# Performance work log

Measured on AMD Instinct MI355X. Metric: run time of the kernel, lower is better.

Reference implementation:

```python
import jax, jax.numpy as jnp
import numpy as np

H = 32  # hidden_size

def _lstm_cell(x, h, c, Wih, Whh, bih, bhh):
    # PyTorch LSTMCell: gates order i, f, g, o
    g = x @ Wih.T + bih + h @ Whh.T + bhh  # [B, 4H]
    i, f, gg, o = jnp.split(g, 4, axis=-1)
    i = jax.nn.sigmoid(i); f = jax.nn.sigmoid(f)
    gg = jnp.tanh(gg);     o = jax.nn.sigmoid(o)
    c_new = f * c + i * gg
    h_new = o * jnp.tanh(c_new)
    return h_new, c_new


def setup_inputs() -> dict:
    key = jax.random.key(0)
    ks = jax.random.split(key, 16)
    B, T, I = 16384, 32, 27
    s_ih0 = 1.0 / np.sqrt(H)
    inp = {
        "obscured_tensor": jax.random.uniform(ks[0], (B, T, I), dtype=jnp.float32),
        "guessed_tensor": jax.random.uniform(ks[1], (B, 26), dtype=jnp.float32),
        # init_state uses xavier_normal on [B,H]: std = sqrt(2/(B+H))
        "h0": jax.random.normal(ks[2], (B, H), dtype=jnp.float32) * np.sqrt(2.0 / (B + H)),
        "c0": jax.random.normal(ks[3], (B, H), dtype=jnp.float32) * np.sqrt(2.0 / (B + H)),
        # layer 0 LSTMCell params (uniform(-1/sqrt(H), 1/sqrt(H)) like torch)
        "Wih0": jax.random.uniform(ks[4], (4 * H, I), jnp.float32, -s_ih0, s_ih0),
        "Whh0": jax.random.uniform(ks[5], (4 * H, H), jnp.float32, -s_ih0, s_ih0),
        "bih0": jax.random.uniform(ks[6], (4 * H,), jnp.float32, -s_ih0, s_ih0),
        "bhh0": jax.random.uniform(ks[7], (4 * H,), jnp.float32, -s_ih0, s_ih0),
        # layer 1 LSTMCell params
        "Wih1": jax.random.uniform(ks[8], (4 * H, H), jnp.float32, -s_ih0, s_ih0),
        "Whh1": jax.random.uniform(ks[9], (4 * H, H), jnp.float32, -s_ih0, s_ih0),
        "bih1": jax.random.uniform(ks[10], (4 * H,), jnp.float32, -s_ih0, s_ih0),
        "bhh1": jax.random.uniform(ks[11], (4 * H,), jnp.float32, -s_ih0, s_ih0),
        # fc: Linear(H + 26, 26)
        "Wfc": jax.random.uniform(ks[12], (26, H + 26), jnp.float32, -1.0 / np.sqrt(H + 26), 1.0 / np.sqrt(H + 26)),
        "bfc": jax.random.uniform(ks[13], (26,), jnp.float32, -1.0 / np.sqrt(H + 26), 1.0 / np.sqrt(H + 26)),
    }
    return inp


def reference(obscured_tensor, guessed_tensor, h0, c0,
              Wih0, Whh0, bih0, bhh0, Wih1, Whh1, bih1, bhh1, Wfc, bfc):
    B, T, _ = obscured_tensor.shape
    # faithful to torch: .view(T, B, -1) is a raw reshape, not a transpose
    xs = obscured_tensor.reshape(T, B, -1)  # [T, B, 27]

    def step(carry, x):
        h1, c1, h2, c2, hsum = carry
        h1, c1 = _lstm_cell(x, h1, c1, Wih0, Whh0, bih0, bhh0)
        h2, c2 = _lstm_cell(h1, h2, c2, Wih1, Whh1, bih1, bhh1)
        return (h1, c1, h2, c2, hsum + h2), None

    # init_state aliases the same xavier-initialized tensor for all layers
    init = (h0, c0, h0, c0, jnp.zeros_like(h0))
    (h1, c1, h2, c2, hsum), _ = jax.lax.scan(step, init, xs)

    # 'avg' aggregation: mean over time of concat(h_top, guessed);
    # guessed is time-constant so mean(concat) == concat(mean(h), guessed)
    agg = jnp.concatenate([hsum / T, guessed_tensor], axis=1)  # [B, H+26]
    logits = agg @ Wfc.T + bfc
    return logits, jax.nn.sigmoid(logits)
```

## Files before the change

### kernel.cpp

```cpp
#include <hip/hip_runtime.h>
#include <hip/hip_bf16.h>

#define NB 16384
#define NT 32
#define NI 27
#define NH 32
#define NG 26

typedef __attribute__((ext_vector_type(8))) short bf16x8;
typedef __attribute__((ext_vector_type(4))) float f32x4;
typedef __attribute__((ext_vector_type(4))) int   i32x4;

#define MFMA(a, b, c) __builtin_amdgcn_mfma_f32_16x16x32_bf16((a), (b), (c), 0, 0, 0)

static __device__ __forceinline__ int pack2(float lo, float hi) {
    unsigned short a = __builtin_bit_cast(unsigned short, __float2bfloat16(lo));
    unsigned short b = __builtin_bit_cast(unsigned short, __float2bfloat16(hi));
    return (int)(((unsigned)b << 16) | (unsigned)a);
}

static __device__ __forceinline__ float sigm(float x) {
    return __builtin_amdgcn_rcpf(1.0f + __expf(-x));
}
static __device__ __forceinline__ float tanh_(float x) {
    return 2.0f * __builtin_amdgcn_rcpf(1.0f + __expf(-2.0f * x)) - 1.0f;
}

static __device__ __forceinline__ bf16x8 load_wfrag(const float* __restrict__ W,
                                                    int rowlen, int nrows, int row, int k0) {
    int w[4];
#pragma unroll
    for (int q = 0; q < 4; ++q) {
        int k = k0 + 2 * q;
        float lo = (row < nrows && k     < rowlen) ? W[row * rowlen + k]     : 0.0f;
        float hi = (row < nrows && k + 1 < rowlen) ? W[row * rowlen + k + 1] : 0.0f;
        w[q] = pack2(lo, hi);
    }
    i32x4 v = { w[0], w[1], w[2], w[3] };
    return __builtin_bit_cast(bf16x8, v);
}

static __device__ __forceinline__ bf16x8 redist(const float hn[4][2], int a0, int a1, bool mhi) {
    int w00 = pack2(hn[0][0], hn[1][0]);
    int w01 = pack2(hn[2][0], hn[3][0]);
    int w10 = pack2(hn[0][1], hn[1][1]);
    int w11 = pack2(hn[2][1], hn[3][1]);
    int q0lo = __builtin_amdgcn_ds_bpermute(a0, w00), q0hi = __builtin_amdgcn_ds_bpermute(a0, w10);
    int q1lo = __builtin_amdgcn_ds_bpermute(a0, w01), q1hi = __builtin_amdgcn_ds_bpermute(a0, w11);
    int q2lo = __builtin_amdgcn_ds_bpermute(a1, w00), q2hi = __builtin_amdgcn_ds_bpermute(a1, w10);
    int q3lo = __builtin_amdgcn_ds_bpermute(a1, w01), q3hi = __builtin_amdgcn_ds_bpermute(a1, w11);
    i32x4 v = { mhi ? q0hi : q0lo, mhi ? q1hi : q1lo, mhi ? q2hi : q2lo, mhi ? q3hi : q3lo };
    return __builtin_bit_cast(bf16x8, v);
}

__global__ __launch_bounds__(256, 1)
void lstm_mfma(const float* __restrict__ X,
               const float* __restrict__ Gu,
               const float* __restrict__ H0, const float* __restrict__ C0,
               const float* __restrict__ Wih0, const float* __restrict__ Whh0,
               const float* __restrict__ bih0, const float* __restrict__ bhh0,
               const float* __restrict__ Wih1, const float* __restrict__ Whh1,
               const float* __restrict__ bih1, const float* __restrict__ bhh1,
               const float* __restrict__ Wfc, const float* __restrict__ bfc,
               float* __restrict__ out)
{
    const int lane = threadIdx.x & 63;
    const int bl   = lane & 15;
    const int g4   = lane >> 4;
    const int k0   = 8 * g4;
    const int wid  = blockIdx.x * (blockDim.x >> 6) + (threadIdx.x >> 6);
    const int batch = wid * 16 + bl;
    const bool mhi = (g4 >> 1) != 0;
    const int a0 = 4 * (bl + 16 * (2 * (g4 & 1)));
    const int a1 = a0 + 64;

    bf16x8 A0x[8], A0h[8], A1i[8], A1h[8];
    f32x4  b0[8], b1[8];
#pragma unroll
    for (int m = 0; m < 8; ++m) {
        A0x[m] = load_wfrag(Wih0, NI, 4 * NH, 16 * m + bl, k0);
        A0h[m] = load_wfrag(Whh0, NH, 4 * NH, 16 * m + bl, k0);
        A1i[m] = load_wfrag(Wih1, NH, 4 * NH, 16 * m + bl, k0);
        A1h[m] = load_wfrag(Whh1, NH, 4 * NH, 16 * m + bl, k0);
#pragma unroll
        for (int r = 0; r < 4; ++r) {
            int gr = 16 * m + 4 * g4 + r;
            b0[m][r] = bih0[gr] + bhh0[gr];
            b1[m][r] = bih1[gr] + bhh1[gr];
        }
    }
    bf16x8 Afc0[2], Afc1[2];
#pragma unroll
    for (int m2 = 0; m2 < 2; ++m2) {
        Afc0[m2] = load_wfrag(Wfc, NH + NG, NG, 16 * m2 + bl, k0);
        Afc1[m2] = load_wfrag(Wfc, NH + NG, NG, 16 * m2 + bl, NH + k0);
    }

    const float* h0p = H0 + (size_t)batch * NH;
    const float* c0p = C0 + (size_t)batch * NH;
    int hw[4];
#pragma unroll
    for (int q = 0; q < 4; ++q) hw[q] = pack2(h0p[k0 + 2 * q], h0p[k0 + 2 * q + 1]);
    i32x4 hv = { hw[0], hw[1], hw[2], hw[3] };
    bf16x8 h1f = __builtin_bit_cast(bf16x8, hv);
    bf16x8 h2f = h1f;
    float c1[4][2], c2[4][2], hsum[4][2];
#pragma unroll
    for (int mh = 0; mh < 2; ++mh)
#pragma unroll
        for (int r = 0; r < 4; ++r) {
            float c = c0p[16 * mh + 4 * g4 + r];
            c1[r][mh] = c; c2[r][mh] = c; hsum[r][mh] = 0.0f;
        }

    float xn[8];
    {
        const float* xp = X + ((size_t)0 * NB + batch) * NI;
#pragma unroll
        for (int j = 0; j < 8; ++j) { int k = k0 + j; xn[j] = (k < NI) ? xp[k] : 0.0f; }
    }

#pragma unroll 1
    for (int t = 0; t < NT; ++t) {
        int xw[4];
#pragma unroll
        for (int q = 0; q < 4; ++q) xw[q] = pack2(xn[2 * q], xn[2 * q + 1]);
        i32x4 xv = { xw[0], xw[1], xw[2], xw[3] };
        bf16x8 xf = __builtin_bit_cast(bf16x8, xv);
        if (t + 1 < NT) {
            const float* xp = X + ((size_t)(t + 1) * NB + batch) * NI;
#pragma unroll
            for (int j = 0; j < 8; ++j) { int k = k0 + j; xn[j] = (k < NI) ? xp[k] : 0.0f; }
        }

        f32x4 g[8];
#pragma unroll
        for (int m = 0; m < 8; ++m) g[m] = MFMA(A0x[m], xf, b0[m]);
#pragma unroll
        for (int m = 0; m < 8; ++m) g[m] = MFMA(A0h[m], h1f, g[m]);
        float hn1[4][2];
#pragma unroll
        for (int mh = 0; mh < 2; ++mh)
#pragma unroll
            for (int r = 0; r < 4; ++r) {
                float iv = sigm(g[0 + mh][r]);
                float fv = sigm(g[2 + mh][r]);
                float gv = tanh_(g[4 + mh][r]);
                float ov = sigm(g[6 + mh][r]);
                float c  = fmaf(fv, c1[r][mh], iv * gv);
                c1[r][mh] = c;
                hn1[r][mh] = ov * tanh_(c);
            }
        h1f = redist(hn1, a0, a1, mhi);

#pragma unroll
        for (int m = 0; m < 8; ++m) g[m] = MFMA(A1i[m], h1f, b1[m]);
#pragma unroll
        for (int m = 0; m < 8; ++m) g[m] = MFMA(A1h[m], h2f, g[m]);
        float hn2[4][2];
#pragma unroll
        for (int mh = 0; mh < 2; ++mh)
#pragma unroll
            for (int r = 0; r < 4; ++r) {
                float iv = sigm(g[0 + mh][r]);
                float fv = sigm(g[2 + mh][r]);
                float gv = tanh_(g[4 + mh][r]);
                float ov = sigm(g[6 + mh][r]);
                float c  = fmaf(fv, c2[r][mh], iv * gv);
                c2[r][mh] = c;
                float h = ov * tanh_(c);
                hn2[r][mh] = h;
                hsum[r][mh] += h;
            }
        h2f = redist(hn2, a0, a1, mhi);
    }

    float hs[4][2];
#pragma unroll
    for (int mh = 0; mh < 2; ++mh)
#pragma unroll
        for (int r = 0; r < 4; ++r) hs[r][mh] = hsum[r][mh] * (1.0f / NT);
    bf16x8 hsf = redist(hs, a0, a1, mhi);

    int gw[4];
    {
        const float* gp = Gu + (size_t)batch * NG;
#pragma unroll
        for (int q = 0; q < 4; ++q) {
            int k = k0 + 2 * q;
            float lo = (k     < NG) ? gp[k]     : 0.0f;
            float hi = (k + 1 < NG) ? gp[k + 1] : 0.0f;
            gw[q] = pack2(lo, hi);
        }
    }
    i32x4 gv_ = { gw[0], gw[1], gw[2], gw[3] };
    bf16x8 guf = __builtin_bit_cast(bf16x8, gv_);

    f32x4 zero4 = { 0.0f, 0.0f, 0.0f, 0.0f };
    f32x4 L[2];
#pragma unroll
    for (int m2 = 0; m2 < 2; ++m2) L[m2] = MFMA(Afc0[m2], hsf, zero4);
#pragma unroll
    for (int m2 = 0; m2 < 2; ++m2) L[m2] = MFMA(Afc1[m2], guf, L[m2]);

#pragma unroll
    for (int m2 = 0; m2 < 2; ++m2)
#pragma unroll
        for (int r = 0; r < 4; ++r) {
            int row = 16 * m2 + 4 * g4 + r;
            if (row < NG) {
                float v = L[m2][r] + bfc[row];
                out[(size_t)batch * NG + row] = v;
                out[(size_t)NB * NG + (size_t)batch * NG + row] = sigm(v);
            }
        }
}

extern "C" void kernel_launch(void* const* d_in, const int* in_sizes, int n_in,
                              void* d_out, int out_size, void* d_ws, size_t ws_size,
                              hipStream_t stream) {
    const float* X    = (const float*)d_in[0];
    const float* Gu   = (const float*)d_in[1];
    const float* H0   = (const float*)d_in[2];
    const float* C0   = (const float*)d_in[3];
    const float* Wih0 = (const float*)d_in[4];
    const float* Whh0 = (const float*)d_in[5];
    const float* bih0 = (const float*)d_in[6];
    const float* bhh0 = (const float*)d_in[7];
    const float* Wih1 = (const float*)d_in[8];
    const float* Whh1 = (const float*)d_in[9];
    const float* bih1 = (const float*)d_in[10];
    const float* bhh1 = (const float*)d_in[11];
    const float* Wfc  = (const float*)d_in[12];
    const float* bfc  = (const float*)d_in[13];
    float* out = (float*)d_out;

    dim3 grid(NB / 16 / 4), block(256);
    hipLaunchKernelGGL(lstm_mfma, grid, block, 0, stream,
                       X, Gu, H0, C0, Wih0, Whh0, bih0, bhh0,
                       Wih1, Whh1, bih1, bhh1, Wfc, bfc, out);
}
```

Measured before the change: 77.47 us.

## Permute weight K-columns to drop bpermute redistribution and fuse gate reciprocals

After: 72.58 us. 6.3% less time.

```diff
diff --git a/kernel.cpp b/kernel.cpp
--- a/kernel.cpp
+++ b/kernel.cpp
@@ -19,50 +19,39 @@
     return (int)(((unsigned)b << 16) | (unsigned)a);
 }
 
-static __device__ __forceinline__ float sigm(float x) {
-    return __builtin_amdgcn_rcpf(1.0f + __expf(-x));
-}
-static __device__ __forceinline__ float tanh_(float x) {
-    return 2.0f * __builtin_amdgcn_rcpf(1.0f + __expf(-2.0f * x)) - 1.0f;
-}
-
 static __device__ __forceinline__ bf16x8 load_wfrag(const float* __restrict__ W,
-                                                    int rowlen, int nrows, int row, int k0) {
+                                                    int rowlen, int nrows, int row,
+                                                    int g4, int kbase, bool perm) {
     int w[4];
 #pragma unroll
     for (int q = 0; q < 4; ++q) {
-        int k = k0 + 2 * q;
-        float lo = (row < nrows && k     < rowlen) ? W[row * rowlen + k]     : 0.0f;
-        float hi = (row < nrows && k + 1 < rowlen) ? W[row * rowlen + k + 1] : 0.0f;
+        int klo = perm ? (16 * (q >> 1) + 4 * g4 + ((2 * q) & 3))
+                       : (kbase + 8 * g4 + 2 * q);
+        int khi = klo + 1;
+        float lo = (row < nrows && klo < rowlen) ? W[row * rowlen + klo] : 0.0f;
+        float hi = (row < nrows && khi < rowlen) ? W[row * rowlen + khi] : 0.0f;
         w[q] = pack2(lo, hi);
     }
     i32x4 v = { w[0], w[1], w[2], w[3] };
     return __builtin_bit_cast(bf16x8, v);
 }
 
-static __device__ __forceinline__ bf16x8 redist(const float hn[4][2], int a0, int a1, bool mhi) {
-    int w00 = pack2(hn[0][0], hn[1][0]);
-    int w01 = pack2(hn[2][0], hn[3][0]);
-    int w10 = pack2(hn[0][1], hn[1][1]);
-    int w11 = pack2(hn[2][1], hn[3][1]);
-    int q0lo = __builtin_amdgcn_ds_bpermute(a0, w00), q0hi = __builtin_amdgcn_ds_bpermute(a0, w10);
-    int q1lo = __builtin_amdgcn_ds_bpermute(a0, w01), q1hi = __builtin_amdgcn_ds_bpermute(a0, w11);
-    int q2lo = __builtin_amdgcn_ds_bpermute(a1, w00), q2hi = __builtin_amdgcn_ds_bpermute(a1, w10);
-    int q3lo = __builtin_amdgcn_ds_bpermute(a1, w01), q3hi = __builtin_amdgcn_ds_bpermute(a1, w11);
-    i32x4 v = { mhi ? q0hi : q0lo, mhi ? q1hi : q1lo, mhi ? q2hi : q2lo, mhi ? q3hi : q3lo };
+static __device__ __forceinline__ bf16x8 pack_bfrag(const float hn[4][2]) {
+    i32x4 v = { pack2(hn[0][0], hn[1][0]), pack2(hn[2][0], hn[3][0]),
+                pack2(hn[0][1], hn[1][1]), pack2(hn[2][1], hn[3][1]) };
     return __builtin_bit_cast(bf16x8, v);
 }
 
 __global__ __launch_bounds__(256, 1)
-void lstm_mfma(const float* __restrict__ X,
-               const float* __restrict__ Gu,
-               const float* __restrict__ H0, const float* __restrict__ C0,
-               const float* __restrict__ Wih0, const float* __restrict__ Whh0,
-               const float* __restrict__ bih0, const float* __restrict__ bhh0,
-               const float* __restrict__ Wih1, const float* __restrict__ Whh1,
-               const float* __restrict__ bih1, const float* __restrict__ bhh1,
-               const float* __restrict__ Wfc, const float* __restrict__ bfc,
-               float* __restrict__ out)
+void lstm_pi(const float* __restrict__ X,
+             const float* __restrict__ Gu,
+             const float* __restrict__ H0, const float* __restrict__ C0,
+             const float* __restrict__ Wih0, const float* __restrict__ Whh0,
+             const float* __restrict__ bih0, const float* __restrict__ bhh0,
+             const float* __restrict__ Wih1, const float* __restrict__ Whh1,
+             const float* __restrict__ bih1, const float* __restrict__ bhh1,
+             const float* __restrict__ Wfc, const float* __restrict__ bfc,
+             float* __restrict__ out)
 {
     const int lane = threadIdx.x & 63;
     const int bl   = lane & 15;
@@ -70,18 +59,15 @@
     const int k0   = 8 * g4;
     const int wid  = blockIdx.x * (blockDim.x >> 6) + (threadIdx.x >> 6);
     const int batch = wid * 16 + bl;
-    const bool mhi = (g4 >> 1) != 0;
-    const int a0 = 4 * (bl + 16 * (2 * (g4 & 1)));
-    const int a1 = a0 + 64;
 
     bf16x8 A0x[8], A0h[8], A1i[8], A1h[8];
     f32x4  b0[8], b1[8];
 #pragma unroll
     for (int m = 0; m < 8; ++m) {
-        A0x[m] = load_wfrag(Wih0, NI, 4 * NH, 16 * m + bl, k0);
-        A0h[m] = load_wfrag(Whh0, NH, 4 * NH, 16 * m + bl, k0);
-        A1i[m] = load_wfrag(Wih1, NH, 4 * NH, 16 * m + bl, k0);
-        A1h[m] = load_wfrag(Whh1, NH, 4 * NH, 16 * m + bl, k0);
+        A0x[m] = load_wfrag(Wih0, NI, 4 * NH, 16 * m + bl, g4, 0, false);
+        A0h[m] = load_wfrag(Whh0, NH, 4 * NH, 16 * m + bl, g4, 0, true);
+        A1i[m] = load_wfrag(Wih1, NH, 4 * NH, 16 * m + bl, g4, 0, true);
+        A1h[m] = load_wfrag(Whh1, NH, 4 * NH, 16 * m + bl, g4, 0, true);
 #pragma unroll
         for (int r = 0; r < 4; ++r) {
             int gr = 16 * m + 4 * g4 + r;
@@ -92,16 +78,18 @@
     bf16x8 Afc0[2], Afc1[2];
 #pragma unroll
     for (int m2 = 0; m2 < 2; ++m2) {
-        Afc0[m2] = load_wfrag(Wfc, NH + NG, NG, 16 * m2 + bl, k0);
-        Afc1[m2] = load_wfrag(Wfc, NH + NG, NG, 16 * m2 + bl, NH + k0);
+        Afc0[m2] = load_wfrag(Wfc, NH + NG, NG, 16 * m2 + bl, g4, 0, true);
+        Afc1[m2] = load_wfrag(Wfc, NH + NG, NG, 16 * m2 + bl, g4, NH, false);
     }
 
     const float* h0p = H0 + (size_t)batch * NH;
     const float* c0p = C0 + (size_t)batch * NH;
-    int hw[4];
-#pragma unroll
-    for (int q = 0; q < 4; ++q) hw[q] = pack2(h0p[k0 + 2 * q], h0p[k0 + 2 * q + 1]);
-    i32x4 hv = { hw[0], hw[1], hw[2], hw[3] };
+    {
+    }
+    i32x4 hv = { pack2(h0p[4 * g4],      h0p[4 * g4 + 1]),
+                 pack2(h0p[4 * g4 + 2],  h0p[4 * g4 + 3]),
+                 pack2(h0p[16 + 4 * g4], h0p[16 + 4 * g4 + 1]),
+                 pack2(h0p[16 + 4 * g4 + 2], h0p[16 + 4 * g4 + 3]) };
     bf16x8 h1f = __builtin_bit_cast(bf16x8, hv);
     bf16x8 h2f = h1f;
     float c1[4][2], c2[4][2], hsum[4][2];
@@ -115,7 +103,7 @@
 
     float xn[8];
     {
-        const float* xp = X + ((size_t)0 * NB + batch) * NI;
+        const float* xp = X + (size_t)batch * NI;
 #pragma unroll
         for (int j = 0; j < 8; ++j) { int k = k0 + j; xn[j] = (k < NI) ? xp[k] : 0.0f; }
     }
@@ -143,15 +131,18 @@
         for (int mh = 0; mh < 2; ++mh)
 #pragma unroll
             for (int r = 0; r < 4; ++r) {
-                float iv = sigm(g[0 + mh][r]);
-                float fv = sigm(g[2 + mh][r]);
-                float gv = tanh_(g[4 + mh][r]);
-                float ov = sigm(g[6 + mh][r]);
-                float c  = fmaf(fv, c1[r][mh], iv * gv);
+                float ei = __expf(-g[0 + mh][r]);
+                float ef = __expf(-g[2 + mh][r]);
+                float eg = __expf(-2.0f * g[4 + mh][r]);
+                float eo = __expf(-g[6 + mh][r]);
+                float ig = (1.0f - eg) * __builtin_amdgcn_rcpf(fmaf(ei, eg, ei) + eg + 1.0f);
+                float fv = __builtin_amdgcn_rcpf(1.0f + ef);
+                float c  = fmaf(fv, c1[r][mh], ig);
                 c1[r][mh] = c;
-                hn1[r][mh] = ov * tanh_(c);
+                float ec = __expf(-2.0f * c);
+                hn1[r][mh] = (1.0f - ec) * __builtin_amdgcn_rcpf(fmaf(eo, ec, eo) + ec + 1.0f);
             }
-        h1f = redist(hn1, a0, a1, mhi);
+        h1f = pack_bfrag(hn1);
 
 #pragma unroll
         for (int m = 0; m < 8; ++m) g[m] = MFMA(A1i[m], h1f, b1[m]);
@@ -162,17 +153,20 @@
         for (int mh = 0; mh < 2; ++mh)
 #pragma unroll
             for (int r = 0; r < 4; ++r) {
-                float iv = sigm(g[0 + mh][r]);
-                float fv = sigm(g[2 + mh][r]);
-                float gv = tanh_(g[4 + mh][r]);
-                float ov = sigm(g[6 + mh][r]);
-                float c  = fmaf(fv, c2[r][mh], iv * gv);
+                float ei = __expf(-g[0 + mh][r]);
+                float ef = __expf(-g[2 + mh][r]);
+                float eg = __expf(-2.0f * g[4 + mh][r]);
+                float eo = __expf(-g[6 + mh][r]);
+                float ig = (1.0f - eg) * __builtin_amdgcn_rcpf(fmaf(ei, eg, ei) + eg + 1.0f);
+                float fv = __builtin_amdgcn_rcpf(1.0f + ef);
+                float c  = fmaf(fv, c2[r][mh], ig);
                 c2[r][mh] = c;
-                float h = ov * tanh_(c);
+                float ec = __expf(-2.0f * c);
+                float h  = (1.0f - ec) * __builtin_amdgcn_rcpf(fmaf(eo, ec, eo) + ec + 1.0f);
                 hn2[r][mh] = h;
                 hsum[r][mh] += h;
             }
-        h2f = redist(hn2, a0, a1, mhi);
+        h2f = pack_bfrag(hn2);
     }
 
     float hs[4][2];
@@ -180,7 +174,7 @@
     for (int mh = 0; mh < 2; ++mh)
 #pragma unroll
         for (int r = 0; r < 4; ++r) hs[r][mh] = hsum[r][mh] * (1.0f / NT);
-    bf16x8 hsf = redist(hs, a0, a1, mhi);
+    bf16x8 hsf = pack_bfrag(hs);
 
     int gw[4];
     {
@@ -211,7 +205,8 @@
             if (row < NG) {
                 float v = L[m2][r] + bfc[row];
                 out[(size_t)batch * NG + row] = v;
-                out[(size_t)NB * NG + (size_t)batch * NG + row] = sigm(v);
+                out[(size_t)NB * NG + (size_t)batch * NG + row] =
+                    __builtin_amdgcn_rcpf(1.0f + __expf(-v));
             }
         }
 }
@@ -236,7 +231,7 @@
     float* out = (float*)d_out;
 
     dim3 grid(NB / 16 / 4), block(256);
-    hipLaunchKernelGGL(lstm_mfma, grid, block, 0, stream,
+    hipLaunchKernelGGL(lstm_pi, grid, block, 0, stream,
                        X, Gu, H0, C0, Wih0, Whh0, bih0, bhh0,
                        Wih1, Whh1, bih1, bhh1, Wfc, bfc, out);
 }
```
